# Kernel optimization log

Measured on AMD Instinct MI355X. Metric: run time of the kernel, lower is better.

Reference implementation:

```python
import jax, jax.numpy as jnp
import numpy as np

CORR_RADIUS = 4  # matches init corr_radius


def setup_inputs() -> dict:
    key = jax.random.key(0)
    k1, k2 = jax.random.split(key)
    B, C, H, W = 8, 256, 96, 128
    x1 = jax.random.normal(k1, (B, C, H, W), dtype=jnp.float32)
    x2 = jax.random.normal(k2, (B, C, H, W), dtype=jnp.float32)
    return {"x1": x1, "x2": x2}


def reference(x1, x2):
    # Local cost volume: for each of the (2r+1)^2 displacements, the
    # unfolded tensor that the torch version builds.
    B, C, H, W = x1.shape
    r = CORR_RADIUS
    D = 2 * r + 1
    x2p = jnp.pad(x2, ((0, 0), (0, 0), (r, r), (r, r)))  # [B,C,H+2r,W+2r]
    inv_c = jnp.asarray(1.0 / C, dtype=x1.dtype)
    outs = []
    for di in range(D):          # small fixed displacement set (9x9)
        for dj in range(D):
            shifted = x2p[:, :, di:di + H, dj:dj + W]  # [B,C,H,W]
            outs.append(jnp.einsum('bchw,bchw->bhw', x1, shifted) * inv_c)
    # torch ordering: unfold over H first then W -> row-major over (di,dj)
    return jnp.stack(outs, axis=1)  # [B, D*D, H, W]
```

## Files before the change

kernel.cpp:

```cpp
#include <hip/hip_runtime.h>

#define Cc 256
#define Hh 96
#define Ww 128
#define CH_STRIDE (Hh * Ww)
#define ROWS 16
#define SCOLS 24
#define ACOLS 32
#define CSL  48
#define UNITS 3

typedef __attribute__((ext_vector_type(8))) short bf16x8;
typedef __attribute__((ext_vector_type(4))) float f32x4;

static __device__ __forceinline__ unsigned cvt_pk(float lo, float hi) {
  unsigned r;
  asm("v_cvt_pk_bf16_f32 %0, %1, %2" : "=v"(r) : "v"(lo), "v"(hi));
  return r;
}

__global__ __launch_bounds__(512)
void corr_mfma(const float* __restrict__ x1, const float* __restrict__ x2,
               float* __restrict__ out) {
  __shared__ __align__(16) unsigned short x2s[ROWS * ACOLS * CSL];

  const int tid  = threadIdx.x;
  const int bid  = blockIdx.x;
  const int sbid = (bid & 7) * 96 + (bid >> 3);

  const int wt  = sbid & 7;
  const int hgb = sbid >> 3;
  const int hg  = hgb % 12;
  const int b   = hgb / 12;
  const int h0  = hg * 8;
  const int w0  = wt * 16;

  const int wv   = tid >> 6;
  const int lane = tid & 63;
  const int n16  = lane & 15;
  const int kgrp = lane >> 4;
  const int h    = h0 + wv;

  const float* uptr[UNITS];
  int  uoff[UNITS];
  bool uok[UNITS];
#pragma unroll
  for (int s = 0; s < UNITS; ++s) {
    const int u   = tid + 512 * s;
    const int chg = u / 384;
    const int rem = u - chg * 384;
    const int r   = rem / SCOLS;
    const int c   = rem - r * SCOLS;
    const int gh  = h0 - 4 + r;
    const int gw  = w0 - 4 + c;
    uok[s] = (gh >= 0) & (gh < Hh) & (gw >= 0) & (gw < Ww);
    const int ghc = uok[s] ? gh : 0;
    const int gwc = uok[s] ? gw : 0;
    uptr[s] = x2 + ((size_t)(b * Cc + chg * 8) * Hh + ghc) * Ww + gwc;
    uoff[s] = (r * ACOLS + c) * CSL + chg * 8;
  }

  const float* pA = x1 + ((size_t)b * Cc * Hh + h) * Ww + (w0 + n16)
                       + (size_t)kgrp * 8 * CH_STRIDE;

  f32x4 acc[9][2];
#pragma unroll
  for (int di = 0; di < 9; ++di)
#pragma unroll
    for (int t = 0; t < 2; ++t) acc[di][t] = (f32x4){0.f, 0.f, 0.f, 0.f};

  float pf[UNITS][8];
#pragma unroll
  for (int s = 0; s < UNITS; ++s)
#pragma unroll
    for (int j = 0; j < 8; ++j)
      pf[s][j] = uok[s] ? uptr[s][(size_t)j * CH_STRIDE] : 0.f;

  for (int ci = 0; ci < 8; ++ci) {
    const int c0 = ci * 32;
    __syncthreads();

    float pa[8];
    {
      const float* pAc = pA + (size_t)c0 * CH_STRIDE;
#pragma unroll
      for (int j = 0; j < 8; ++j) pa[j] = pAc[(size_t)j * CH_STRIDE];
    }

#pragma unroll
    for (int s = 0; s < UNITS; ++s) {
      uint4 pk;
      pk.x = cvt_pk(pf[s][0], pf[s][1]);
      pk.y = cvt_pk(pf[s][2], pf[s][3]);
      pk.z = cvt_pk(pf[s][4], pf[s][5]);
      pk.w = cvt_pk(pf[s][6], pf[s][7]);
      *(uint4*)(&x2s[uoff[s]]) = pk;
    }

    bf16x8 af;
    {
      union { unsigned u[4]; bf16x8 v; } ux;
      ux.u[0] = cvt_pk(pa[0], pa[1]);
      ux.u[1] = cvt_pk(pa[2], pa[3]);
      ux.u[2] = cvt_pk(pa[4], pa[5]);
      ux.u[3] = cvt_pk(pa[6], pa[7]);
      af = ux.v;
    }

    if (ci < 7) {
      const size_t nb = (size_t)(c0 + 32) * CH_STRIDE;
#pragma unroll
      for (int s = 0; s < UNITS; ++s)
#pragma unroll
        for (int j = 0; j < 8; ++j)
          pf[s][j] = uok[s] ? uptr[s][nb + (size_t)j * CH_STRIDE] : 0.f;
    }

    __syncthreads();

#pragma unroll
    for (int di = 0; di < 9; ++di) {
      const int r = wv + di;
#pragma unroll
      for (int t = 0; t < 2; ++t) {
        const bf16x8 bf_ =
            *(const bf16x8*)(&x2s[(r * ACOLS + 16 * t + n16) * CSL + kgrp * 8]);
        acc[di][t] = __builtin_amdgcn_mfma_f32_16x16x32_bf16(af, bf_, acc[di][t], 0, 0, 0);
      }
    }
  }

  const float scale = 1.0f / (float)Cc;
#pragma unroll
  for (int di = 0; di < 9; ++di) {
#pragma unroll
    for (int t = 0; t < 2; ++t) {
#pragma unroll
      for (int q = 0; q < 4; ++q) {
        const int m  = kgrp * 4 + q;
        const int dj = 16 * t + n16 - m;
        if (dj >= 0 && dj <= 8) {
          out[(((size_t)b * 81 + di * 9 + dj) * Hh + h) * Ww + (w0 + m)]
              = acc[di][t][q] * scale;
        }
      }
    }
  }
}

extern "C" void kernel_launch(void* const* d_in, const int* in_sizes, int n_in,
                              void* d_out, int out_size, void* d_ws, size_t ws_size,
                              hipStream_t stream) {
  const float* x1 = (const float*)d_in[0];
  const float* x2 = (const float*)d_in[1];
  float* out = (float*)d_out;
  corr_mfma<<<768, 512, 0, stream>>>(x1, x2, out);
}
```

Before: 66.06 us.

## Deepen global prefetch to two stages and shrink LDS channel padding

The channel loop is unrolled by two with separate even/odd register buffers, so x2 loads are issued two chunks ahead and x1 loads one chunk ahead. This gives more time to hide global memory latency before the values are written to LDS. The LDS channel stride is also reduced from 48 to 40 elements, which changes the bank mapping and shrinks shared memory. The extra prefetch buffers raise register pressure, which may reduce occupancy or cause spills at 512 threads per block.

```diff
diff --git a/kernel.cpp b/kernel.cpp
--- a/kernel.cpp
+++ b/kernel.cpp
@@ -7,7 +7,7 @@
 #define ROWS 16
 #define SCOLS 24
 #define ACOLS 32
-#define CSL  48
+#define CSL  40
 #define UNITS 3
 
 typedef __attribute__((ext_vector_type(8))) short bf16x8;
@@ -18,6 +18,61 @@
   asm("v_cvt_pk_bf16_f32 %0, %1, %2" : "=v"(r) : "v"(lo), "v"(hi));
   return r;
 }
+
+#define PF_LOAD(pf, cx)                                               \
+  do {                                                                \
+    const size_t cb_ = (size_t)(cx) * 32 * CH_STRIDE;                 \
+    _Pragma("unroll")                                                 \
+    for (int s = 0; s < UNITS; ++s)                                   \
+      _Pragma("unroll")                                               \
+      for (int j = 0; j < 8; ++j)                                     \
+        pf[s][j] = uok[s] ? uptr[s][cb_ + (size_t)j * CH_STRIDE] : 0.f; \
+  } while (0)
+
+#define LDS_WRITE(pf)                                                 \
+  do {                                                                \
+    _Pragma("unroll")                                                 \
+    for (int s = 0; s < UNITS; ++s) {                                 \
+      uint4 pk;                                                       \
+      pk.x = cvt_pk(pf[s][0], pf[s][1]);                              \
+      pk.y = cvt_pk(pf[s][2], pf[s][3]);                              \
+      pk.z = cvt_pk(pf[s][4], pf[s][5]);                              \
+      pk.w = cvt_pk(pf[s][6], pf[s][7]);                              \
+      *(uint4*)(&x2s[uoff[s]]) = pk;                                  \
+    }                                                                 \
+  } while (0)
+
+#define A_LOAD(pa, cx)                                                \
+  do {                                                                \
+    const float* pAc_ = pA + (size_t)(cx) * 32 * CH_STRIDE;           \
+    _Pragma("unroll")                                                 \
+    for (int j = 0; j < 8; ++j) pa[j] = pAc_[(size_t)j * CH_STRIDE];  \
+  } while (0)
+
+#define COMPUTE(af)                                                   \
+  do {                                                                \
+    _Pragma("unroll")                                                 \
+    for (int di = 0; di < 9; ++di) {                                  \
+      const int r_ = wv + di;                                         \
+      _Pragma("unroll")                                               \
+      for (int t = 0; t < 2; ++t) {                                   \
+        const bf16x8 bf_ = *(const bf16x8*)(                          \
+            &x2s[(r_ * ACOLS + 16 * t + n16) * CSL + kgrp * 8]);      \
+        acc[di][t] = __builtin_amdgcn_mfma_f32_16x16x32_bf16(         \
+            af, bf_, acc[di][t], 0, 0, 0);                            \
+      }                                                               \
+    }                                                                 \
+  } while (0)
+
+#define AFRAG(af, pa)                                                 \
+  do {                                                                \
+    union { unsigned u[4]; bf16x8 v; } ux_;                           \
+    ux_.u[0] = cvt_pk(pa[0], pa[1]);                                  \
+    ux_.u[1] = cvt_pk(pa[2], pa[3]);                                  \
+    ux_.u[2] = cvt_pk(pa[4], pa[5]);                                  \
+    ux_.u[3] = cvt_pk(pa[6], pa[7]);                                  \
+    af = ux_.v;                                                       \
+  } while (0)
 
 __global__ __launch_bounds__(512)
 void corr_mfma(const float* __restrict__ x1, const float* __restrict__ x2,
@@ -69,65 +124,28 @@
 #pragma unroll
     for (int t = 0; t < 2; ++t) acc[di][t] = (f32x4){0.f, 0.f, 0.f, 0.f};
 
-  float pf[UNITS][8];
-#pragma unroll
-  for (int s = 0; s < UNITS; ++s)
-#pragma unroll
-    for (int j = 0; j < 8; ++j)
-      pf[s][j] = uok[s] ? uptr[s][(size_t)j * CH_STRIDE] : 0.f;
+  float pfE[UNITS][8], pfO[UNITS][8], pa[8];
+  PF_LOAD(pfE, 0);
+  PF_LOAD(pfO, 1);
+  A_LOAD(pa, 0);
 
-  for (int ci = 0; ci < 8; ++ci) {
-    const int c0 = ci * 32;
+  for (int ci = 0; ci < 8; ci += 2) {
     __syncthreads();
-
-    float pa[8];
-    {
-      const float* pAc = pA + (size_t)c0 * CH_STRIDE;
-#pragma unroll
-      for (int j = 0; j < 8; ++j) pa[j] = pAc[(size_t)j * CH_STRIDE];
-    }
-
-#pragma unroll
-    for (int s = 0; s < UNITS; ++s) {
-      uint4 pk;
-      pk.x = cvt_pk(pf[s][0], pf[s][1]);
-      pk.y = cvt_pk(pf[s][2], pf[s][3]);
-      pk.z = cvt_pk(pf[s][4], pf[s][5]);
-      pk.w = cvt_pk(pf[s][6], pf[s][7]);
-      *(uint4*)(&x2s[uoff[s]]) = pk;
-    }
-
+    LDS_WRITE(pfE);
     bf16x8 af;
-    {
-      union { unsigned u[4]; bf16x8 v; } ux;
-      ux.u[0] = cvt_pk(pa[0], pa[1]);
-      ux.u[1] = cvt_pk(pa[2], pa[3]);
-      ux.u[2] = cvt_pk(pa[4], pa[5]);
-      ux.u[3] = cvt_pk(pa[6], pa[7]);
-      af = ux.v;
-    }
-
-    if (ci < 7) {
-      const size_t nb = (size_t)(c0 + 32) * CH_STRIDE;
-#pragma unroll
-      for (int s = 0; s < UNITS; ++s)
-#pragma unroll
-        for (int j = 0; j < 8; ++j)
-          pf[s][j] = uok[s] ? uptr[s][nb + (size_t)j * CH_STRIDE] : 0.f;
-    }
+    AFRAG(af, pa);
+    A_LOAD(pa, ci + 1);
+    if (ci < 6) PF_LOAD(pfE, ci + 2);
+    __syncthreads();
+    COMPUTE(af);
 
     __syncthreads();
-
-#pragma unroll
-    for (int di = 0; di < 9; ++di) {
-      const int r = wv + di;
-#pragma unroll
-      for (int t = 0; t < 2; ++t) {
-        const bf16x8 bf_ =
-            *(const bf16x8*)(&x2s[(r * ACOLS + 16 * t + n16) * CSL + kgrp * 8]);
-        acc[di][t] = __builtin_amdgcn_mfma_f32_16x16x32_bf16(af, bf_, acc[di][t], 0, 0, 0);
-      }
-    }
+    LDS_WRITE(pfO);
+    AFRAG(af, pa);
+    if (ci < 6) A_LOAD(pa, ci + 2);
+    if (ci < 5) PF_LOAD(pfO, ci + 3);
+    __syncthreads();
+    COMPUTE(af);
   }
 
   const float scale = 1.0f / (float)Cc;
```

Measured after the change: 71.35 us. +8.0%, slower.

## Stage x2 tile with float4 loads and swizzle LDS channel slots

Applied to the files above, without the earlier changes.

The x2 halo tile is now staged by 384 threads that each issue 8 float4 global loads covering 4 adjacent columns, replacing 3 units × 8 scalar loads per thread. This cuts load instruction count and improves coalescing. The bf16 channel-group slot in LDS is XOR-style rotated by row, and the MFMA B-operand reads use the matching slot, to reduce LDS bank conflicts. Idle threads 384..511 no longer stage, which concentrates staging work on fewer waves.

```diff
diff --git a/kernel.cpp b/kernel.cpp
--- a/kernel.cpp
+++ b/kernel.cpp
@@ -8,7 +8,6 @@
 #define SCOLS 24
 #define ACOLS 32
 #define CSL  48
-#define UNITS 3
 
 typedef __attribute__((ext_vector_type(8))) short bf16x8;
 typedef __attribute__((ext_vector_type(4))) float f32x4;
@@ -18,6 +17,30 @@
   asm("v_cvt_pk_bf16_f32 %0, %1, %2" : "=v"(r) : "v"(lo), "v"(hi));
   return r;
 }
+
+#define FCOMP(v, cc) ((cc) == 0 ? (v).x : (cc) == 1 ? (v).y : (cc) == 2 ? (v).z : (v).w)
+
+#define PF_LOAD(pf, cx)                                               \
+  do {                                                                \
+    const size_t cb_ = (size_t)(cx) * 32 * CH_STRIDE;                 \
+    _Pragma("unroll")                                                 \
+    for (int j = 0; j < 8; ++j)                                       \
+      pf[j] = sok ? *(const float4*)(sptr + cb_ + (size_t)j * CH_STRIDE) \
+                  : make_float4(0.f, 0.f, 0.f, 0.f);                  \
+  } while (0)
+
+#define LDS_WRITE(pf)                                                 \
+  do {                                                                \
+    _Pragma("unroll")                                                 \
+    for (int cc = 0; cc < 4; ++cc) {                                  \
+      uint4 pk;                                                       \
+      pk.x = cvt_pk(FCOMP(pf[0], cc), FCOMP(pf[1], cc));              \
+      pk.y = cvt_pk(FCOMP(pf[2], cc), FCOMP(pf[3], cc));              \
+      pk.z = cvt_pk(FCOMP(pf[4], cc), FCOMP(pf[5], cc));              \
+      pk.w = cvt_pk(FCOMP(pf[6], cc), FCOMP(pf[7], cc));              \
+      *(uint4*)(&x2s[soff + cc * CSL]) = pk;                          \
+    }                                                                 \
+  } while (0)
 
 __global__ __launch_bounds__(512)
 void corr_mfma(const float* __restrict__ x1, const float* __restrict__ x2,
@@ -41,24 +64,17 @@
   const int kgrp = lane >> 4;
   const int h    = h0 + wv;
 
-  const float* uptr[UNITS];
-  int  uoff[UNITS];
-  bool uok[UNITS];
-#pragma unroll
-  for (int s = 0; s < UNITS; ++s) {
-    const int u   = tid + 512 * s;
-    const int chg = u / 384;
-    const int rem = u - chg * 384;
-    const int r   = rem / SCOLS;
-    const int c   = rem - r * SCOLS;
-    const int gh  = h0 - 4 + r;
-    const int gw  = w0 - 4 + c;
-    uok[s] = (gh >= 0) & (gh < Hh) & (gw >= 0) & (gw < Ww);
-    const int ghc = uok[s] ? gh : 0;
-    const int gwc = uok[s] ? gw : 0;
-    uptr[s] = x2 + ((size_t)(b * Cc + chg * 8) * Hh + ghc) * Ww + gwc;
-    uoff[s] = (r * ACOLS + c) * CSL + chg * 8;
-  }
+  const bool stager = (tid < 384);
+  const int ug   = tid % 6;
+  const int ur   = (tid / 6) % 16;
+  const int uchg = tid / 96;
+  const int gh   = h0 - 4 + ur;
+  const int gw0  = w0 - 4 + 4 * ug;
+  const bool sok = stager & (gh >= 0) & (gh < Hh) & (gw0 >= 0) & (gw0 + 3 < Ww);
+  const int ghc  = sok ? gh : 0;
+  const int gwc  = sok ? gw0 : 0;
+  const float* sptr = x2 + ((size_t)(b * Cc + uchg * 8) * Hh + ghc) * Ww + gwc;
+  const int soff = (ur * ACOLS + 4 * ug) * CSL + (((uchg + ur) & 3) << 3);
 
   const float* pA = x1 + ((size_t)b * Cc * Hh + h) * Ww + (w0 + n16)
                        + (size_t)kgrp * 8 * CH_STRIDE;
@@ -69,33 +85,20 @@
 #pragma unroll
     for (int t = 0; t < 2; ++t) acc[di][t] = (f32x4){0.f, 0.f, 0.f, 0.f};
 
-  float pf[UNITS][8];
-#pragma unroll
-  for (int s = 0; s < UNITS; ++s)
-#pragma unroll
-    for (int j = 0; j < 8; ++j)
-      pf[s][j] = uok[s] ? uptr[s][(size_t)j * CH_STRIDE] : 0.f;
+  float4 pf[8];
+  if (stager) PF_LOAD(pf, 0);
 
   for (int ci = 0; ci < 8; ++ci) {
-    const int c0 = ci * 32;
     __syncthreads();
 
     float pa[8];
     {
-      const float* pAc = pA + (size_t)c0 * CH_STRIDE;
+      const float* pAc = pA + (size_t)(ci * 32) * CH_STRIDE;
 #pragma unroll
       for (int j = 0; j < 8; ++j) pa[j] = pAc[(size_t)j * CH_STRIDE];
     }
 
-#pragma unroll
-    for (int s = 0; s < UNITS; ++s) {
-      uint4 pk;
-      pk.x = cvt_pk(pf[s][0], pf[s][1]);
-      pk.y = cvt_pk(pf[s][2], pf[s][3]);
-      pk.z = cvt_pk(pf[s][4], pf[s][5]);
-      pk.w = cvt_pk(pf[s][6], pf[s][7]);
-      *(uint4*)(&x2s[uoff[s]]) = pk;
-    }
+    if (stager) LDS_WRITE(pf);
 
     bf16x8 af;
     {
@@ -107,24 +110,18 @@
       af = ux.v;
     }
 
-    if (ci < 7) {
-      const size_t nb = (size_t)(c0 + 32) * CH_STRIDE;
-#pragma unroll
-      for (int s = 0; s < UNITS; ++s)
-#pragma unroll
-        for (int j = 0; j < 8; ++j)
-          pf[s][j] = uok[s] ? uptr[s][nb + (size_t)j * CH_STRIDE] : 0.f;
-    }
+    if (stager && ci < 7) PF_LOAD(pf, ci + 1);
 
     __syncthreads();
 
 #pragma unroll
     for (int di = 0; di < 9; ++di) {
-      const int r = wv + di;
+      const int r_ = wv + di;
+      const int slot = ((kgrp + r_) & 3) << 3;
 #pragma unroll
       for (int t = 0; t < 2; ++t) {
         const bf16x8 bf_ =
-            *(const bf16x8*)(&x2s[(r * ACOLS + 16 * t + n16) * CSL + kgrp * 8]);
+            *(const bf16x8*)(&x2s[(r_ * ACOLS + 16 * t + n16) * CSL + slot]);
         acc[di][t] = __builtin_amdgcn_mfma_f32_16x16x32_bf16(af, bf_, acc[di][t], 0, 0, 0);
       }
     }
```

New measurement: 62.69 us. 1.05x faster.
